# Kernel tuning notes

Measured on AMD Instinct MI355X. Metric: run time of the kernel, lower is better.

## Reference

```python
import jax, jax.numpy as jnp
import numpy as np

B, CZ, E, V, H, W = 256, 512, 512, 4096, 16, 16  # batch, z_channels, embed_dim, vocab, latent HxW


def setup_inputs() -> dict:
    key = jax.random.key(0)
    k0, k1, k2, k3 = jax.random.split(key, 4)
    x = jax.random.normal(k0, (B, CZ, H, W), jnp.float32)          # encoder feature map
    pre_w = jax.random.normal(k1, (E, CZ), jnp.float32) * 0.02     # 1x1 pre_quant_conv weight
    pre_b = jnp.zeros((E,), jnp.float32)
    emb = jax.random.uniform(k2, (V, E), jnp.float32, -1.0 / V, 1.0 / V)  # codebook, uniform init as in module
    post_w = jax.random.normal(k3, (CZ, E), jnp.float32) * 0.02    # 1x1 post_quant_conv weight
    post_b = jnp.zeros((CZ,), jnp.float32)
    return dict(x=x, pre_w=pre_w, pre_b=pre_b, emb=emb, post_w=post_w, post_b=post_b)


def reference(x, pre_w, pre_b, emb, post_w, post_b):
    # pre_quant_conv: 1x1 Conv2d(CZ -> E)
    z = jnp.einsum('bchw,ec->behw', x, pre_w) + pre_b[None, :, None, None]
    b, e, h, w = z.shape
    # flatten spatial: (b h w, e)
    zf = z.transpose(0, 2, 3, 1).reshape(-1, e)
    # expanded squared-distance to codebook: ||z||^2 + ||c||^2 - 2 z.c
    dist = (jnp.sum(zf * zf, axis=1, keepdims=True)
            + jnp.sum(emb * emb, axis=1)
            - 2.0 * zf @ emb.T)                                    # [bhw, V]
    tokens = jnp.argmin(dist, axis=-1)                             # [bhw] int
    z_q = emb[tokens].reshape(b, h, w, e).transpose(0, 3, 1, 2)    # gather -> [b,e,h,w]
    # straight-through estimator
    dec_in = z + jax.lax.stop_gradient(z_q - z)
    # post_quant_conv: 1x1 Conv2d(E -> CZ)
    rec = jnp.einsum('behw,ce->bchw', dec_in, post_w) + post_b[None, :, None, None]
    return z, z_q, rec
```

## Files before the change

kernel.cpp:

```cpp
#include <hip/hip_runtime.h>
#include <hip/hip_bf16.h>

typedef unsigned short u16;
typedef unsigned char  u8;
typedef unsigned int   u32;
typedef unsigned long long u64;

using short8 = __attribute__((ext_vector_type(8))) short;
using f32x4  = __attribute__((ext_vector_type(4))) float;
using u16x8  = __attribute__((ext_vector_type(8))) unsigned short;
using ll2    = __attribute__((ext_vector_type(2))) long long;

#define AS_GLOBAL __attribute__((address_space(1)))
#define AS_LDS    __attribute__((address_space(3)))

__device__ __forceinline__ u16 f2b(float x){
  u32 u = __float_as_uint(x);
  u32 r = (u + 0x7FFFu + ((u >> 16) & 1u)) >> 16;
  return (u16)r;
}
__device__ __forceinline__ float b2f(u16 h){ return __uint_as_float(((u32)h) << 16); }

__device__ __forceinline__ u32 f2e4m3(float x){
  float ax = fabsf(x);
  u32 s = (__float_as_uint(x) & 0x80000000u) >> 24;
  ax = fminf(ax, 448.0f);
  if (ax < 0.015625f){
    u32 m = (u32)__float2int_rn(ax * 512.0f);
    return s | m;
  }
  u32 u = __float_as_uint(ax);
  u32 man = u & 0x7FFFFFu;
  u32 rnd = man + 0x7FFFFu + ((man >> 20) & 1u);
  u32 e = (u >> 23) + (rnd >> 23);
  u32 m = (rnd >> 23) ? 0u : ((rnd >> 20) & 7u);
  if (e > 135u) return s | 0x7Eu;
  return s | ((e - 120u) << 3) | m;
}

__device__ __forceinline__ void gload16(u16* l, const u16* g){
  __builtin_amdgcn_global_load_lds((const AS_GLOBAL u32*)g, (AS_LDS u32*)l, 16, 0, 0);
}

__device__ __forceinline__ u64 umin64(u64 a, u64 b){ return a < b ? a : b; }

__device__ __forceinline__ u64 shfl_xor_u64(u64 v, int m){
  u32 lo = __shfl_xor((u32)v, m, 64);
  u32 hi = __shfl_xor((u32)(v >> 32), m, 64);
  return ((u64)hi << 32) | lo;
}

__global__ void k_prep(const float* __restrict__ x,
                       const float* __restrict__ pre_w,
                       const float* __restrict__ post_w,
                       const float* __restrict__ emb,
                       u16* __restrict__ xb, u16* __restrict__ prew_b,
                       u16* __restrict__ postw_b, u16* __restrict__ emb_b,
                       u8* __restrict__ emb8, float* __restrict__ cn26){
  __shared__ float t[64][65];
  const int bid = blockIdx.x;
  const int tid = threadIdx.x;

  if (bid < 8192){
    const int b  = bid >> 5;
    const int rb = (bid >> 2) & 7;
    const int cb = bid & 3;
    const float* s = x + ((size_t)b * 512 + (size_t)rb * 64) * 256 + cb * 64;
    #pragma unroll
    for (int j = 0; j < 4; ++j){
      int fl = j * 256 + tid;
      int r = fl >> 4, c4 = (fl & 15) * 4;
      float4 v = *(const float4*)(s + (size_t)r * 256 + c4);
      t[r][c4 + 0] = v.x; t[r][c4 + 1] = v.y; t[r][c4 + 2] = v.z; t[r][c4 + 3] = v.w;
    }
    __syncthreads();
    u16* o = xb + ((size_t)b * 256 + (size_t)cb * 64) * 512 + rb * 64;
    #pragma unroll
    for (int j = 0; j < 2; ++j){
      int fl = j * 256 + tid;
      int c = fl >> 3, r8 = (fl & 7) * 8;
      u16x8 hv;
      #pragma unroll
      for (int i = 0; i < 8; ++i) hv[i] = f2b(t[r8 + i][c]);
      *(u16x8*)(o + (size_t)c * 512 + r8) = hv;
    }
  } else if (bid < 9216){
    int i = (bid - 8192) * 256 + tid;
    prew_b[i] = f2b(pre_w[i]);
  } else if (bid < 10240){
    int i = (bid - 9216) * 256 + tid;
    postw_b[i] = f2b(post_w[i]);
  } else if (bid < 18432){
    int i = (bid - 10240) * 256 + tid;
    emb_b[i] = f2b(emb[i]);
  } else if (bid < 20480){
    int id = (bid - 18432) * 256 + tid;
    int row = id >> 7, db = id & 127;
    int b0 = db * 4;
    int kb = b0 >> 6, r6 = b0 & 63;
    int g = r6 >> 4, ks = (r6 >> 3) & 1, j0 = r6 & 7;
    int k = kb * 64 + ks * 32 + g * 8 + j0;
    const float* p = emb + (size_t)row * 512 + k;
    u32 w = f2e4m3(p[0] * 1048576.0f)
          | (f2e4m3(p[1] * 1048576.0f) << 8)
          | (f2e4m3(p[2] * 1048576.0f) << 16)
          | (f2e4m3(p[3] * 1048576.0f) << 24);
    *(u32*)(emb8 + (size_t)row * 512 + b0) = w;
  } else {
    int wv = tid >> 6, lane = tid & 63;
    int v = (bid - 20480) * 4 + wv;
    const float* r = emb + (size_t)v * 512;
    float s = 0.f;
    #pragma unroll
    for (int i = 0; i < 8; ++i){ float xx = r[lane + i * 64]; s += xx * xx; }
    #pragma unroll
    for (int off = 32; off; off >>= 1) s += __shfl_down(s, off, 64);
    if (lane == 0) cn26[v] = s * 67108864.0f;
  }
}

template<int MODE>
__global__ __launch_bounds__(256, 4) void k_gemm(
    const u16* __restrict__ Ah,
    const u16* __restrict__ Bh,
    const u64* __restrict__ gkeys,
    const float* __restrict__ bias,
    float* __restrict__ Cout,
    u8* __restrict__ Z8,
    int M, int mtbits)
{
  constexpr int K = 512;
  __shared__ __align__(16) u16 sA[128 * 64];
  __shared__ __align__(16) u16 sB[128 * 64];

  const int tid  = threadIdx.x;
  const int lane = tid & 63;
  const int wid  = tid >> 6;
  const int wm = wid >> 1, wn = wid & 1;

  const int nwg = gridDim.x;
  const int chunk = nwg >> 3;
  const int pb = blockIdx.x;
  const int bid = (pb & 7) * chunk + (pb >> 3);

  const int mt = bid & ((1 << mtbits) - 1);
  const int nt = (bid >> mtbits) & 1;
  const int b  = bid >> (mtbits + 1);
  const int m0 = mt * 128;
  const int n0 = nt * 128;
  const int bbase = b * 256;

  const u16* ga[4];
  const u16* gb[4];
  int ldso[4];
  #pragma unroll
  for (int i = 0; i < 4; ++i){
    int e = i * 256 + tid;
    int r = e >> 3;
    int sl = (e & 7) ^ (r & 7);
    ldso[i] = e * 8;
    ga[i] = Ah + (size_t)(m0 + r) * K + sl * 8;
    size_t brow;
    if (MODE == 2) brow = (size_t)(u32)gkeys[bbase + n0 + r];
    else           brow = (size_t)(bbase + n0 + r);
    gb[i] = Bh + brow * K + sl * 8;
  }

  const f32x4 zero4 = {0.f, 0.f, 0.f, 0.f};
  f32x4 acc[4][4];
  #pragma unroll
  for (int i = 0; i < 4; ++i)
    #pragma unroll
    for (int j = 0; j < 4; ++j) acc[i][j] = zero4;

  int aoff[2][4], boff[2][4];
  #pragma unroll
  for (int ks = 0; ks < 2; ++ks)
    #pragma unroll
    for (int f = 0; f < 4; ++f){
      int rA = wm * 64 + f * 16 + (lane & 15);
      aoff[ks][f] = rA * 64 + (((ks * 4 + (lane >> 4)) ^ (rA & 7)) * 8);
      int rB = wn * 64 + f * 16 + (lane & 15);
      boff[ks][f] = rB * 64 + (((ks * 4 + (lane >> 4)) ^ (rB & 7)) * 8);
    }

  for (int kt = 0; kt < 8; ++kt){
    const int k0 = kt * 64;
    #pragma unroll
    for (int i = 0; i < 4; ++i){
      gload16(&sA[ldso[i]], ga[i] + k0);
      gload16(&sB[ldso[i]], gb[i] + k0);
    }
    __syncthreads();
    #pragma unroll
    for (int ks = 0; ks < 2; ++ks){
      short8 ah[4], bh[4];
      #pragma unroll
      for (int f = 0; f < 4; ++f){
        ah[f] = *(const short8*)&sA[aoff[ks][f]];
        bh[f] = *(const short8*)&sB[boff[ks][f]];
      }
      #pragma unroll
      for (int fm = 0; fm < 4; ++fm)
        #pragma unroll
        for (int fn = 0; fn < 4; ++fn)
          acc[fm][fn] = __builtin_amdgcn_mfma_f32_16x16x32_bf16(ah[fm], bh[fn], acc[fm][fn], 0, 0, 0);
    }
    __syncthreads();
  }

  const int row0 = m0 + wm * 64;
  const int col  = n0 + wn * 64 + (lane & 15);
  float* Cb = Cout + (size_t)b * M * 256;
  #pragma unroll
  for (int fm = 0; fm < 4; ++fm){
    #pragma unroll
    for (int j = 0; j < 4; ++j){
      int row = row0 + fm * 16 + (lane >> 4) * 4 + j;
      float bi = bias[row];
      #pragma unroll
      for (int fn = 0; fn < 4; ++fn)
        Cb[(size_t)row * 256 + col + fn * 16] = acc[fm][fn][j] + bi;
    }
  }

  if (MODE == 0){
    #pragma unroll
    for (int fm = 0; fm < 4; ++fm){
      int rb4 = row0 + fm * 16 + (lane >> 4) * 4;
      int pb0 = (rb4 >> 6) * 64 + (((rb4 >> 3) & 3) * 16) + (((rb4 >> 5) & 1) * 8) + (rb4 & 7);
      float bi0 = bias[rb4], bi1 = bias[rb4+1], bi2 = bias[rb4+2], bi3 = bias[rb4+3];
      #pragma unroll
      for (int fn = 0; fn < 4; ++fn){
        u32 w = f2e4m3((acc[fm][fn][0] + bi0) * 64.0f)
              | (f2e4m3((acc[fm][fn][1] + bi1) * 64.0f) << 8)
              | (f2e4m3((acc[fm][fn][2] + bi2) * 64.0f) << 16)
              | (f2e4m3((acc[fm][fn][3] + bi3) * 64.0f) << 24);
        *(u32*)(Z8 + (size_t)(bbase + col + fn * 16) * 512 + pb0) = w;
      }
    }
  }
}

__global__ __launch_bounds__(512, 1) void k_gemm2(
    const u8* __restrict__ A8,
    const u8* __restrict__ B8,
    const float* __restrict__ cn26,
    u64* __restrict__ okeys)
{
  __shared__ __align__(16) u8 lds[163840];

  const int tid  = threadIdx.x;
  const int lane = tid & 63;
  const int wid  = tid >> 6;
  const int wm   = wid >> 2;
  const int wn   = wid & 3;
  const int b    = blockIdx.x;
  const int bbase = b * 256;
  const int g4   = lane >> 4;

#define SB    __builtin_amdgcn_sched_barrier(0)
#define BAR   __builtin_amdgcn_s_barrier()
#define VM2   asm volatile("s_waitcnt vmcnt(2)" ::: "memory")
#define VM0   asm volatile("s_waitcnt vmcnt(0)" ::: "memory")

  #pragma unroll
  for (int i = 0; i < 16; ++i){
    int e = i * 512 + tid;
    int t = e >> 5, s = e & 31;
    gload16((u16*)&lds[e * 16],
            (const u16*)(B8 + (size_t)(bbase + t) * 512 + ((s ^ (t & 31)) * 16)));
  }

  const u8* gsrcA0;
  const u8* gsrcA1;
  {
    int r0 = tid >> 2, s0 = tid & 3;
    int sl0 = (s0 - (r0 >> 1)) & 3;
    gsrcA0 = A8 + (size_t)r0 * 512 + sl0 * 16;
    int r1 = r0 + 128;
    int sl1 = (s0 - (r1 >> 1)) & 3;
    gsrcA1 = A8 + (size_t)r1 * 512 + sl1 * 16;
  }

#define STG_A(tp) { const size_t _o = (size_t)((tp) >> 3) * 131072 + ((tp) & 7) * 64; \
    const int _d = 131072 + (((tp) & 1) * 16384); \
    gload16((u16*)&lds[_d + tid * 16], (const u16*)(gsrcA0 + _o)); \
    gload16((u16*)&lds[_d + 8192 + tid * 16], (const u16*)(gsrcA1 + _o)); }

  int aBase[8];
  #pragma unroll
  for (int fm = 0; fm < 8; ++fm){
    int row = wm * 128 + fm * 16 + (lane & 15);
    int sl = (g4 + ((lane & 15) >> 1)) & 3;
    aBase[fm] = 131072 + row * 64 + sl * 16;
  }
  int tB[4], mB[4];
  #pragma unroll
  for (int fn = 0; fn < 4; ++fn){
    tB[fn] = wn * 64 + fn * 16 + (lane & 15);
    mB[fn] = tB[fn] & 31;
  }

  const f32x4 zero4 = {0.f, 0.f, 0.f, 0.f};
  f32x4 acc[8][4];
  #pragma unroll
  for (int i = 0; i < 8; ++i)
    #pragma unroll
    for (int j = 0; j < 4; ++j) acc[i][j] = zero4;

  u64 best[4];
  #pragma unroll
  for (int i = 0; i < 4; ++i) best[i] = ~0ull;

  STG_A(0)

  for (int mt = 0; mt < 16; ++mt){
    #pragma unroll
    for (int kt = 0; kt < 8; ++kt){
      const int tau = mt * 8 + kt;
      if (tau < 127) STG_A(tau + 1)
      if (tau == 127){ VM0; } else { VM2; }
      SB; BAR; SB;

      const int bufo = (tau & 1) * 16384;
      ll2 af[8], bv[4];
      #pragma unroll
      for (int fm = 0; fm < 8; ++fm)
        af[fm] = *(const ll2*)&lds[aBase[fm] + bufo];
      #pragma unroll
      for (int fn = 0; fn < 4; ++fn)
        bv[fn] = *(const ll2*)&lds[tB[fn] * 512 + (((kt * 4 + g4) ^ mB[fn]) * 16)];

      __builtin_amdgcn_s_setprio(1);
      #pragma unroll
      for (int fm = 0; fm < 8; ++fm)
        #pragma unroll
        for (int fn = 0; fn < 4; ++fn)
          acc[fm][fn] = __builtin_amdgcn_mfma_f32_16x16x32_fp8_fp8(af[fm][0], bv[fn][0], acc[fm][fn], 0, 0, 0);
      #pragma unroll
      for (int fm = 0; fm < 8; ++fm)
        #pragma unroll
        for (int fn = 0; fn < 4; ++fn)
          acc[fm][fn] = __builtin_amdgcn_mfma_f32_16x16x32_fp8_fp8(af[fm][1], bv[fn][1], acc[fm][fn], 0, 0, 0);
      __builtin_amdgcn_s_setprio(0);
      SB; BAR; SB;
    }

    {
      const float4* cp = (const float4*)(cn26 + mt * 256 + wm * 128 + g4 * 4);
      float4 cnr[8];
      #pragma unroll
      for (int fm = 0; fm < 8; ++fm) cnr[fm] = cp[fm * 4];
      VM0;
      #pragma unroll
      for (int fn = 0; fn < 4; ++fn){
        #pragma unroll
        for (int fm = 0; fm < 8; ++fm){
          #pragma unroll
          for (int jj = 0; jj < 4; ++jj){
            int v = mt * 256 + wm * 128 + fm * 16 + g4 * 4 + jj;
            float sc = ((const float*)&cnr[fm])[jj] - 2.0f * acc[fm][fn][jj];
            u32 o = __float_as_uint(sc);
            o = (o & 0x80000000u) ? ~o : (o | 0x80000000u);
            best[fn] = umin64(best[fn], ((u64)o << 32) | (u32)v);
          }
        }
      }
      #pragma unroll
      for (int i = 0; i < 8; ++i)
        #pragma unroll
        for (int jj = 0; jj < 4; ++jj) acc[i][jj] = zero4;
    }
  }

  #pragma unroll
  for (int fn = 0; fn < 4; ++fn){
    best[fn] = umin64(best[fn], shfl_xor_u64(best[fn], 16));
    best[fn] = umin64(best[fn], shfl_xor_u64(best[fn], 32));
  }
  __syncthreads();
  u64* kbuf = (u64*)&lds[131072];
  if (lane < 16){
    #pragma unroll
    for (int fn = 0; fn < 4; ++fn)
      kbuf[wm * 256 + wn * 64 + fn * 16 + lane] = best[fn];
  }
  __syncthreads();
  if (tid < 256)
    okeys[bbase + tid] = umin64(kbuf[tid], kbuf[256 + tid]);

#undef STG_A
#undef SB
#undef BAR
#undef VM2
#undef VM0
}

__global__ __launch_bounds__(256, 4) void k_tail(
    const u16* __restrict__ Ah,
    const u16* __restrict__ Bh,
    const u64* __restrict__ gkeys,
    const float* __restrict__ bias,
    float* __restrict__ Cout,
    const float* __restrict__ emb,
    float* __restrict__ zq)
{
  constexpr int K = 512;
  __shared__ __align__(16) u16 sA[128 * 64];
  __shared__ __align__(16) u16 sB[128 * 64];

  const int tid = threadIdx.x;

  if (blockIdx.x >= 2048){
    int sidx = (blockIdx.x - 2048) * 256 + tid;
    int b = sidx >> 8, s = sidx & 255;
    int v = (int)(u32)gkeys[sidx];
    const float4* er = (const float4*)(emb + (size_t)v * 512);
    float* o = zq + (size_t)b * 512 * 256 + s;
    #pragma unroll 4
    for (int e4 = 0; e4 < 128; ++e4){
      float4 vv = er[e4];
      o[(size_t)(e4 * 4 + 0) * 256] = vv.x;
      o[(size_t)(e4 * 4 + 1) * 256] = vv.y;
      o[(size_t)(e4 * 4 + 2) * 256] = vv.z;
      o[(size_t)(e4 * 4 + 3) * 256] = vv.w;
    }
    return;
  }

  const int lane = tid & 63;
  const int wid  = tid >> 6;
  const int wm = wid >> 1, wn = wid & 1;

  const int chunk = 2048 >> 3;
  const int pb = blockIdx.x;
  const int bid = (pb & 7) * chunk + (pb >> 3);

  const int mt = bid & 3;
  const int nt = (bid >> 2) & 1;
  const int b  = bid >> 3;
  const int m0 = mt * 128;
  const int n0 = nt * 128;
  const int bbase = b * 256;

  const u16* ga[4];
  const u16* gb[4];
  int ldso[4];
  #pragma unroll
  for (int i = 0; i < 4; ++i){
    int e = i * 256 + tid;
    int r = e >> 3;
    int sl = (e & 7) ^ (r & 7);
    ldso[i] = e * 8;
    ga[i] = Ah + (size_t)(m0 + r) * K + sl * 8;
    size_t brow = (size_t)(u32)gkeys[bbase + n0 + r];
    gb[i] = Bh + brow * K + sl * 8;
  }

  const f32x4 zero4 = {0.f, 0.f, 0.f, 0.f};
  f32x4 acc[4][4];
  #pragma unroll
  for (int i = 0; i < 4; ++i)
    #pragma unroll
    for (int j = 0; j < 4; ++j) acc[i][j] = zero4;

  int aoff[2][4], boff[2][4];
  #pragma unroll
  for (int ks = 0; ks < 2; ++ks)
    #pragma unroll
    for (int f = 0; f < 4; ++f){
      int rA = wm * 64 + f * 16 + (lane & 15);
      aoff[ks][f] = rA * 64 + (((ks * 4 + (lane >> 4)) ^ (rA & 7)) * 8);
      int rB = wn * 64 + f * 16 + (lane & 15);
      boff[ks][f] = rB * 64 + (((ks * 4 + (lane >> 4)) ^ (rB & 7)) * 8);
    }

  for (int kt = 0; kt < 8; ++kt){
    const int k0 = kt * 64;
    #pragma unroll
    for (int i = 0; i < 4; ++i){
      gload16(&sA[ldso[i]], ga[i] + k0);
      gload16(&sB[ldso[i]], gb[i] + k0);
    }
    __syncthreads();
    #pragma unroll
    for (int ks = 0; ks < 2; ++ks){
      short8 ah[4], bh[4];
      #pragma unroll
      for (int f = 0; f < 4; ++f){
        ah[f] = *(const short8*)&sA[aoff[ks][f]];
        bh[f] = *(const short8*)&sB[boff[ks][f]];
      }
      #pragma unroll
      for (int fm = 0; fm < 4; ++fm)
        #pragma unroll
        for (int fn = 0; fn < 4; ++fn)
          acc[fm][fn] = __builtin_amdgcn_mfma_f32_16x16x32_bf16(ah[fm], bh[fn], acc[fm][fn], 0, 0, 0);
    }
    __syncthreads();
  }

  const int row0 = m0 + wm * 64;
  const int col  = n0 + wn * 64 + (lane & 15);
  float* Cb = Cout + (size_t)b * K * 256;
  #pragma unroll
  for (int fm = 0; fm < 4; ++fm){
    #pragma unroll
    for (int j = 0; j < 4; ++j){
      int row = row0 + fm * 16 + (lane >> 4) * 4 + j;
      float bi = bias[row];
      #pragma unroll
      for (int fn = 0; fn < 4; ++fn)
        Cb[(size_t)row * 256 + col + fn * 16] = acc[fm][fn][j] + bi;
    }
  }
}

extern "C" void kernel_launch(void* const* d_in, const int* in_sizes, int n_in,
                              void* d_out, int out_size, void* d_ws, size_t ws_size,
                              hipStream_t stream){
  const float* x      = (const float*)d_in[0];
  const float* pre_w  = (const float*)d_in[1];
  const float* pre_b  = (const float*)d_in[2];
  const float* emb    = (const float*)d_in[3];
  const float* post_w = (const float*)d_in[4];
  const float* post_b = (const float*)d_in[5];

  float* z_out   = (float*)d_out;
  float* zq_out  = z_out + 33554432;
  float* rec_out = z_out + 67108864;

  char* w = (char*)d_ws;
  u16* prew_b  = (u16*)(w);
  u16* postw_b = (u16*)(w + 524288);
  u16* emb_b   = (u16*)(w + 1048576);
  u8*  emb8    = (u8*)(w + 5242880);
  float* cn26  = (float*)(w + 7340032);
  u64* keys    = (u64*)(w + 7356416);
  u16* xb      = (u16*)(w + 7880704);
  u8*  z8      = (u8*)(w + 74989568);

  k_prep<<<21504, 256, 0, stream>>>(x, pre_w, post_w, emb,
                                    xb, prew_b, postw_b, emb_b, emb8, cn26);

  k_gemm<0><<<256 * 2 * 4, 256, 0, stream>>>(prew_b, xb,
      nullptr, pre_b, z_out, z8, 512, 2);

  k_gemm2<<<256, 512, 0, stream>>>(emb8, z8, cn26, keys);

  k_tail<<<2048 + 256, 256, 0, stream>>>(postw_b, emb_b, keys, post_b,
                                         rec_out, emb, zq_out);
}
```

Before: 576.3 us.

## Switch fp8 distance GEMM to 32x32x64 scaled MFMA with plain row-major layouts

Replaces the 16x16x32 fp8 MFMA tiles in the codebook-distance kernel with the MI355X 32x32x64 f8f6f4 scaled MFMA, using neutral unit scales. The fp8 codebook and latent buffers are now written in plain row-major order instead of the old swizzled k-permuted layout, and LDS is indexed with k-chunk-major planes. The intent is fewer, larger matrix instructions and simpler addressing. The trade-off is that the XOR swizzle is gone, so LDS bank conflicts may rise, and the argmin epilogue now has to follow the 32x32 accumulator layout.

Result: slower. 932.6 us (+61.8%).

```diff
diff --git a/kernel.cpp b/kernel.cpp
--- a/kernel.cpp
+++ b/kernel.cpp
@@ -8,8 +8,10 @@
 
 using short8 = __attribute__((ext_vector_type(8))) short;
 using f32x4  = __attribute__((ext_vector_type(4))) float;
+using f32x16 = __attribute__((ext_vector_type(16))) float;
 using u16x8  = __attribute__((ext_vector_type(8))) unsigned short;
-using ll2    = __attribute__((ext_vector_type(2))) long long;
+using i32x4  = __attribute__((ext_vector_type(4))) int;
+using i32x8  = __attribute__((ext_vector_type(8))) int;
 
 #define AS_GLOBAL __attribute__((address_space(1)))
 #define AS_LDS    __attribute__((address_space(3)))
@@ -48,6 +50,13 @@
   u32 lo = __shfl_xor((u32)v, m, 64);
   u32 hi = __shfl_xor((u32)(v >> 32), m, 64);
   return ((u64)hi << 32) | lo;
+}
+
+__device__ __forceinline__ i32x8 cat8(i32x4 lo, i32x4 hi){
+  i32x8 r;
+  r[0] = lo[0]; r[1] = lo[1]; r[2] = lo[2]; r[3] = lo[3];
+  r[4] = hi[0]; r[5] = hi[1]; r[6] = hi[2]; r[7] = hi[3];
+  return r;
 }
 
 __global__ void k_prep(const float* __restrict__ x,
@@ -95,17 +104,12 @@
     emb_b[i] = f2b(emb[i]);
   } else if (bid < 20480){
     int id = (bid - 18432) * 256 + tid;
-    int row = id >> 7, db = id & 127;
-    int b0 = db * 4;
-    int kb = b0 >> 6, r6 = b0 & 63;
-    int g = r6 >> 4, ks = (r6 >> 3) & 1, j0 = r6 & 7;
-    int k = kb * 64 + ks * 32 + g * 8 + j0;
-    const float* p = emb + (size_t)row * 512 + k;
+    const float* p = emb + (size_t)id * 4;
     u32 w = f2e4m3(p[0] * 1048576.0f)
           | (f2e4m3(p[1] * 1048576.0f) << 8)
           | (f2e4m3(p[2] * 1048576.0f) << 16)
           | (f2e4m3(p[3] * 1048576.0f) << 24);
-    *(u32*)(emb8 + (size_t)row * 512 + b0) = w;
+    *(u32*)(emb8 + (size_t)id * 4) = w;
   } else {
     int wv = tid >> 6, lane = tid & 63;
     int v = (bid - 20480) * 4 + wv;
@@ -228,7 +232,6 @@
     #pragma unroll
     for (int fm = 0; fm < 4; ++fm){
       int rb4 = row0 + fm * 16 + (lane >> 4) * 4;
-      int pb0 = (rb4 >> 6) * 64 + (((rb4 >> 3) & 3) * 16) + (((rb4 >> 5) & 1) * 8) + (rb4 & 7);
       float bi0 = bias[rb4], bi1 = bias[rb4+1], bi2 = bias[rb4+2], bi3 = bias[rb4+3];
       #pragma unroll
       for (int fn = 0; fn < 4; ++fn){
@@ -236,7 +239,7 @@
               | (f2e4m3((acc[fm][fn][1] + bi1) * 64.0f) << 8)
               | (f2e4m3((acc[fm][fn][2] + bi2) * 64.0f) << 16)
               | (f2e4m3((acc[fm][fn][3] + bi3) * 64.0f) << 24);
-        *(u32*)(Z8 + (size_t)(bbase + col + fn * 16) * 512 + pb0) = w;
+        *(u32*)(Z8 + (size_t)(bbase + col + fn * 16) * 512 + rb4) = w;
       }
     }
   }
@@ -257,7 +260,8 @@
   const int wn   = wid & 3;
   const int b    = blockIdx.x;
   const int bbase = b * 256;
-  const int g4   = lane >> 4;
+  const int lo   = lane & 31;
+  const int hi   = lane >> 5;
 
 #define SB    __builtin_amdgcn_sched_barrier(0)
 #define BAR   __builtin_amdgcn_s_barrier()
@@ -267,51 +271,37 @@
   #pragma unroll
   for (int i = 0; i < 16; ++i){
     int e = i * 512 + tid;
-    int t = e >> 5, s = e & 31;
     gload16((u16*)&lds[e * 16],
-            (const u16*)(B8 + (size_t)(bbase + t) * 512 + ((s ^ (t & 31)) * 16)));
-  }
-
-  const u8* gsrcA0;
-  const u8* gsrcA1;
-  {
-    int r0 = tid >> 2, s0 = tid & 3;
-    int sl0 = (s0 - (r0 >> 1)) & 3;
-    gsrcA0 = A8 + (size_t)r0 * 512 + sl0 * 16;
-    int r1 = r0 + 128;
-    int sl1 = (s0 - (r1 >> 1)) & 3;
-    gsrcA1 = A8 + (size_t)r1 * 512 + sl1 * 16;
-  }
+            (const u16*)(B8 + (size_t)(bbase + (e & 255)) * 512 + (e >> 8) * 16));
+  }
+
+  const u8* gsrcA0 = A8 + (size_t)(tid & 255) * 512 + (tid >> 8) * 16;
+  const u8* gsrcA1 = gsrcA0 + 32;
 
 #define STG_A(tp) { const size_t _o = (size_t)((tp) >> 3) * 131072 + ((tp) & 7) * 64; \
     const int _d = 131072 + (((tp) & 1) * 16384); \
     gload16((u16*)&lds[_d + tid * 16], (const u16*)(gsrcA0 + _o)); \
     gload16((u16*)&lds[_d + 8192 + tid * 16], (const u16*)(gsrcA1 + _o)); }
 
-  int aBase[8];
-  #pragma unroll
-  for (int fm = 0; fm < 8; ++fm){
-    int row = wm * 128 + fm * 16 + (lane & 15);
-    int sl = (g4 + ((lane & 15) >> 1)) & 3;
-    aBase[fm] = 131072 + row * 64 + sl * 16;
-  }
-  int tB[4], mB[4];
-  #pragma unroll
-  for (int fn = 0; fn < 4; ++fn){
-    tB[fn] = wn * 64 + fn * 16 + (lane & 15);
-    mB[fn] = tB[fn] & 31;
-  }
-
-  const f32x4 zero4 = {0.f, 0.f, 0.f, 0.f};
-  f32x4 acc[8][4];
-  #pragma unroll
-  for (int i = 0; i < 8; ++i)
-    #pragma unroll
-    for (int j = 0; j < 4; ++j) acc[i][j] = zero4;
-
-  u64 best[4];
-  #pragma unroll
-  for (int i = 0; i < 4; ++i) best[i] = ~0ull;
+  int aOff[4];
+  #pragma unroll
+  for (int fm = 0; fm < 4; ++fm)
+    aOff[fm] = 131072 + (hi * 2) * 4096 + (wm * 128 + fm * 32 + lo) * 16;
+  int bOff[2];
+  #pragma unroll
+  for (int fnb = 0; fnb < 2; ++fnb)
+    bOff[fnb] = (hi * 2) * 4096 + (wn * 64 + fnb * 32 + lo) * 16;
+
+  f32x16 acc[4][2];
+  #pragma unroll
+  for (int i = 0; i < 4; ++i)
+    #pragma unroll
+    for (int j = 0; j < 2; ++j)
+      #pragma unroll
+      for (int e = 0; e < 16; ++e) acc[i][j][e] = 0.f;
+
+  u64 best[2];
+  best[0] = ~0ull; best[1] = ~0ull;
 
   STG_A(0)
 
@@ -324,67 +314,68 @@
       SB; BAR; SB;
 
       const int bufo = (tau & 1) * 16384;
-      ll2 af[8], bv[4];
-      #pragma unroll
-      for (int fm = 0; fm < 8; ++fm)
-        af[fm] = *(const ll2*)&lds[aBase[fm] + bufo];
-      #pragma unroll
-      for (int fn = 0; fn < 4; ++fn)
-        bv[fn] = *(const ll2*)&lds[tB[fn] * 512 + (((kt * 4 + g4) ^ mB[fn]) * 16)];
+      i32x8 av[4], bvv[2];
+      #pragma unroll
+      for (int fm = 0; fm < 4; ++fm){
+        i32x4 l0 = *(const i32x4*)&lds[aOff[fm] + bufo];
+        i32x4 h0 = *(const i32x4*)&lds[aOff[fm] + bufo + 4096];
+        av[fm] = cat8(l0, h0);
+      }
+      #pragma unroll
+      for (int fnb = 0; fnb < 2; ++fnb){
+        i32x4 l0 = *(const i32x4*)&lds[bOff[fnb] + kt * 16384];
+        i32x4 h0 = *(const i32x4*)&lds[bOff[fnb] + kt * 16384 + 4096];
+        bvv[fnb] = cat8(l0, h0);
+      }
 
       __builtin_amdgcn_s_setprio(1);
       #pragma unroll
-      for (int fm = 0; fm < 8; ++fm)
+      for (int fm = 0; fm < 4; ++fm)
         #pragma unroll
-        for (int fn = 0; fn < 4; ++fn)
-          acc[fm][fn] = __builtin_amdgcn_mfma_f32_16x16x32_fp8_fp8(af[fm][0], bv[fn][0], acc[fm][fn], 0, 0, 0);
-      #pragma unroll
-      for (int fm = 0; fm < 8; ++fm)
-        #pragma unroll
-        for (int fn = 0; fn < 4; ++fn)
-          acc[fm][fn] = __builtin_amdgcn_mfma_f32_16x16x32_fp8_fp8(af[fm][1], bv[fn][1], acc[fm][fn], 0, 0, 0);
+        for (int fnb = 0; fnb < 2; ++fnb)
+          acc[fm][fnb] = __builtin_amdgcn_mfma_scale_f32_32x32x64_f8f6f4(
+              av[fm], bvv[fnb], acc[fm][fnb],
+              0, 0,
+              0, 0x7F7F7F7F,
+              0, 0x7F7F7F7F);
       __builtin_amdgcn_s_setprio(0);
       SB; BAR; SB;
     }
 
-    {
-      const float4* cp = (const float4*)(cn26 + mt * 256 + wm * 128 + g4 * 4);
-      float4 cnr[8];
-      #pragma unroll
-      for (int fm = 0; fm < 8; ++fm) cnr[fm] = cp[fm * 4];
-      VM0;
-      #pragma unroll
-      for (int fn = 0; fn < 4; ++fn){
+    #pragma unroll
+    for (int fm = 0; fm < 4; ++fm){
+      #pragma unroll
+      for (int q = 0; q < 4; ++q){
+        const int v0 = mt * 256 + wm * 128 + fm * 32 + q * 8 + hi * 4;
+        float4 cnr = *(const float4*)(cn26 + v0);
         #pragma unroll
-        for (int fm = 0; fm < 8; ++fm){
+        for (int fnb = 0; fnb < 2; ++fnb){
           #pragma unroll
-          for (int jj = 0; jj < 4; ++jj){
-            int v = mt * 256 + wm * 128 + fm * 16 + g4 * 4 + jj;
-            float sc = ((const float*)&cnr[fm])[jj] - 2.0f * acc[fm][fn][jj];
+          for (int j = 0; j < 4; ++j){
+            float sc = ((const float*)&cnr)[j] - 2.0f * acc[fm][fnb][q * 4 + j];
             u32 o = __float_as_uint(sc);
             o = (o & 0x80000000u) ? ~o : (o | 0x80000000u);
-            best[fn] = umin64(best[fn], ((u64)o << 32) | (u32)v);
+            best[fnb] = umin64(best[fnb], ((u64)o << 32) | (u32)(v0 + j));
           }
         }
       }
-      #pragma unroll
-      for (int i = 0; i < 8; ++i)
+    }
+    VM0;
+    #pragma unroll
+    for (int i = 0; i < 4; ++i)
+      #pragma unroll
+      for (int j = 0; j < 2; ++j)
         #pragma unroll
-        for (int jj = 0; jj < 4; ++jj) acc[i][jj] = zero4;
-    }
-  }
-
-  #pragma unroll
-  for (int fn = 0; fn < 4; ++fn){
-    best[fn] = umin64(best[fn], shfl_xor_u64(best[fn], 16));
-    best[fn] = umin64(best[fn], shfl_xor_u64(best[fn], 32));
-  }
+        for (int e = 0; e < 16; ++e) acc[i][j][e] = 0.f;
+  }
+
+  best[0] = umin64(best[0], shfl_xor_u64(best[0], 32));
+  best[1] = umin64(best[1], shfl_xor_u64(best[1], 32));
   __syncthreads();
   u64* kbuf = (u64*)&lds[131072];
-  if (lane < 16){
-    #pragma unroll
-    for (int fn = 0; fn < 4; ++fn)
-      kbuf[wm * 256 + wn * 64 + fn * 16 + lane] = best[fn];
+  if (lane < 32){
+    kbuf[wm * 256 + wn * 64 + lo]      = best[0];
+    kbuf[wm * 256 + wn * 64 + 32 + lo] = best[1];
   }
   __syncthreads();
   if (tid < 256)
```
